# Kernel tuning notes

Measured on AMD Instinct MI355X. Metric: run time of the kernel, lower is better.

Reference implementation:

```python
import jax, jax.numpy as jnp
import numpy as np

B, L, D, H = 64, 64, 512, 512


def setup_inputs() -> dict:
    key = jax.random.key(0)
    ks = jax.random.split(key, 6)
    x = jax.random.normal(ks[0], (B, L, D), dtype=jnp.float32)
    length = jax.random.randint(ks[1], (B,), L // 2, L + 1)  # in [L/2, L]
    # torch Linear convention: weight (out_features, in_features)
    w_word = jax.random.normal(ks[2], (2 * H, D), dtype=jnp.float32) * (1.0 / np.sqrt(D))
    b_word = jnp.zeros((2 * H,), dtype=jnp.float32)
    w_comp = jax.random.normal(ks[3], (5 * H, 2 * H), dtype=jnp.float32) * (1.0 / np.sqrt(2 * H))
    b_comp = jnp.zeros((5 * H,), dtype=jnp.float32)
    comp_query = jax.random.normal(ks[4], (H,), dtype=jnp.float32) * 0.01
    return {"x": x, "length": length, "w_word": w_word, "b_word": b_word,
            "w_comp": w_comp, "b_comp": b_comp, "comp_query": comp_query}


def _treelstm_cell(hl, cl, hr, cr, w_comp, b_comp):
    v = jnp.concatenate([hl, hr], axis=2) @ w_comp.T + b_comp  # (B, n, 5H)
    i, fl, fr, u, o = jnp.split(v, 5, axis=2)
    c = (cl * jax.nn.sigmoid(fl + 1.0) + cr * jax.nn.sigmoid(fr + 1.0)
         + jnp.tanh(u) * jax.nn.sigmoid(i))
    h = jax.nn.sigmoid(o) * jnp.tanh(c)
    return h, c


def _forward(x, length, w_word, b_word, w_comp, b_comp, comp_query):
    max_depth = x.shape[1]
    hdim = comp_query.shape[0]
    # length_mask[b, t] = t < length[b]
    length_mask = (jnp.arange(max_depth)[None, :] < length[:, None]).astype(x.dtype)
    state = x @ w_word.T + b_word  # (B, L, 2H)
    h, c = jnp.split(state, 2, axis=2)
    NEG = jnp.asarray(-1e9, dtype=x.dtype)
    for i in range(max_depth - 1):
        hl, cl = h[:, :-1, :], c[:, :-1, :]
        hr, cr = h[:, 1:, :], c[:, 1:, :]
        new_h, new_c = _treelstm_cell(hl, cl, hr, cr, w_comp, b_comp)
        if i < max_depth - 2:
            # greedy merge-point selection (eval-mode greedy_select)
            cw = jnp.einsum('bnh,h->bn', new_h, comp_query) / np.sqrt(hdim)
            m = length_mask[:, i + 1:]  # (B, L-1-i)
            logits = jnp.where(m > 0, cw, NEG)
            sel = jax.nn.one_hot(jnp.argmax(logits, axis=1), logits.shape[1], dtype=x.dtype)
            cs = jnp.cumsum(sel, axis=1)
            left = (1.0 - cs)[:, :, None]
            right = (cs - sel)[:, :, None]
            s = sel[:, :, None]
            new_h = s * new_h + left * hl + right * hr
            new_c = s * new_c + left * cl + right * cr
        done = length_mask[:, i + 1][:, None, None]
        h = done * new_h + (1.0 - done) * h[:, :-1, :]
        c = done * new_c + (1.0 - done) * c[:, :-1, :]
    return h[:, 0, :], c[:, 0, :]


def reference(x, length, w_word, b_word, w_comp, b_comp, comp_query):
    return _forward(x, length, w_word, b_word, w_comp, b_comp, comp_query)
```

## Files before the change

kernel.cpp:

```cpp
#include <hip/hip_runtime.h>

typedef __bf16 bf16;
typedef short s16x8 __attribute__((ext_vector_type(8)));
typedef float f32x4 __attribute__((ext_vector_type(4)));
typedef unsigned long long u64;

#define MFMA16(a, b, c) __builtin_amdgcn_mfma_f32_16x16x32_bf16((a), (b), (c), 0, 0, 0)
#define NROW 187
#define UROW 251

__device__ __forceinline__ float sigf(float x) { return 1.0f / (1.0f + expf(-x)); }
__device__ __forceinline__ s16x8 ld8(const bf16* p) { return *(const s16x8*)p; }

__device__ __forceinline__ unsigned packhl(float v) {
    bf16 h = (bf16)v;
    bf16 l = (bf16)(v - (float)h);
    return (unsigned)__builtin_bit_cast(unsigned short, h) |
           ((unsigned)__builtin_bit_cast(unsigned short, l) << 16);
}
__device__ __forceinline__ u64 lda64(const unsigned* p) {
    return __hip_atomic_load((const u64*)p, __ATOMIC_RELAXED, __HIP_MEMORY_SCOPE_AGENT);
}
__device__ __forceinline__ u64 lda64u(const u64* p) {
    return __hip_atomic_load(p, __ATOMIC_RELAXED, __HIP_MEMORY_SCOPE_AGENT);
}
__device__ __forceinline__ void stau64(u64* p, u64 v) {
    __hip_atomic_store(p, v, __ATOMIC_RELAXED, __HIP_MEMORY_SCOPE_AGENT);
}
__device__ __forceinline__ unsigned lda32(const unsigned* p) {
    return __hip_atomic_load(p, __ATOMIC_RELAXED, __HIP_MEMORY_SCOPE_AGENT);
}
__device__ __forceinline__ float ldaf(const float* p) {
    return __hip_atomic_load(p, __ATOMIC_RELAXED, __HIP_MEMORY_SCOPE_AGENT);
}
__device__ __forceinline__ void staf(float* p, float v) {
    __hip_atomic_store(p, v, __ATOMIC_RELAXED, __HIP_MEMORY_SCOPE_AGENT);
}
__device__ __forceinline__ void stau(unsigned* p, unsigned v) {
    __hip_atomic_store(p, v, __ATOMIC_RELAXED, __HIP_MEMORY_SCOPE_AGENT);
}

__device__ bf16  g_xhi[64 * 64 * 512], g_xlo[64 * 64 * 512];
__device__ bf16  g_wwhi[1024 * 512], g_wwlo[1024 * 512];
__device__ bf16  g_wchi[2560 * 1024], g_wclo[2560 * 1024];
__device__ bf16  g_hhi[64 * 64 * 512];
__device__ bf16  g_hlo[64 * 64 * 512];
__device__ unsigned g_uhl[(size_t)64 * UROW * 512];
__device__ float g_uc[(size_t)64 * UROW * 512];
__device__ float g_spinit[64 * 63 * 32];
__device__ u64   g_spart2[2 * 128 * 32];
__device__ unsigned g_flag[63 * 8 * 32];

__global__ __launch_bounds__(256) void k_prep(const float* __restrict__ x,
                                              const float* __restrict__ ww,
                                              const float* __restrict__ wc) {
    const int NX = 64 * 64 * 512, NW = 1024 * 512, NC = 2560 * 1024;
    int stride = gridDim.x * 256, i0 = blockIdx.x * 256 + threadIdx.x;
    for (int i = i0; i < NX; i += stride) {
        float v = x[i];
        bf16 h = (bf16)v;
        g_xhi[i] = h;
        g_xlo[i] = (bf16)(v - (float)h);
    }
    for (int i = i0; i < NW; i += stride) {
        float v = ww[i];
        bf16 h = (bf16)v;
        g_wwhi[i] = h;
        g_wwlo[i] = (bf16)(v - (float)h);
    }
    for (int i = i0; i < NC; i += stride) {
        float v = wc[i];
        bf16 h = (bf16)v;
        g_wchi[i] = h;
        g_wclo[i] = (bf16)(v - (float)h);
    }
}

__global__ __launch_bounds__(64) void k_leaf(const float* __restrict__ b_word) {
    int cg = blockIdx.x, rg = blockIdx.y;
    int lane = threadIdx.x, l15 = lane & 15, quad = lane >> 4;
    const bf16* axh = g_xhi + (size_t)(rg * 16 + l15) * 512;
    const bf16* axl = g_xlo + (size_t)(rg * 16 + l15) * 512;
    const bf16* bwh = g_wwhi + (size_t)(cg * 64 + l15) * 512;
    const bf16* bwl = g_wwlo + (size_t)(cg * 64 + l15) * 512;
    f32x4 acc[4] = {};
    for (int kc = 0; kc < 16; ++kc) {
        int k = kc * 32 + quad * 8;
        s16x8 aH = ld8(axh + k), aL = ld8(axl + k);
#pragma unroll
        for (int t = 0; t < 4; ++t) {
            s16x8 bH = ld8(bwh + (size_t)t * 16 * 512 + k);
            s16x8 bL = ld8(bwl + (size_t)t * 16 * 512 + k);
            acc[t] = MFMA16(aH, bH, acc[t]);
            acc[t] = MFMA16(aH, bL, acc[t]);
            acc[t] = MFMA16(aL, bH, acc[t]);
        }
    }
#pragma unroll
    for (int t = 0; t < 4; ++t) {
        int col = cg * 64 + t * 16 + l15;
        float bw = b_word[col];
#pragma unroll
        for (int r = 0; r < 4; ++r) {
            int m = rg * 16 + quad * 4 + r;
            int bb = m >> 6, sl = m & 63;
            float v = acc[t][r] + bw;
            if (col < 512) {
                bf16 hi = (bf16)v;
                g_hhi[(size_t)m * 512 + col] = hi;
                g_hlo[(size_t)m * 512 + col] = (bf16)(v - (float)hi);
                g_uhl[((size_t)bb * UROW + sl) * 512 + col] = packhl(v);
            } else {
                g_uc[((size_t)bb * UROW + sl) * 512 + (col - 512)] = v;
            }
        }
    }
}

__global__ __launch_bounds__(64) void k_cells_init(const int* __restrict__ length,
                                                   const float* __restrict__ b_comp,
                                                   const float* __restrict__ q) {
    int fg = blockIdx.x;
    int rg = blockIdx.y;
    int lane = threadIdx.x, l15 = lane & 15, quad = lane >> 4;

    const bf16 *ahi[4], *alo[4];
#pragma unroll
    for (int t = 0; t < 4; ++t) {
        int r = rg * 64 + t * 16 + l15;
        int b = r / 63, j = r - b * 63;
        ahi[t] = g_hhi + (size_t)(b * 64 + j) * 512;
        alo[t] = g_hlo + (size_t)(b * 64 + j) * 512;
    }
    const bf16* wh = g_wchi + (size_t)(fg * 16 + l15) * 1024;
    const bf16* wl = g_wclo + (size_t)(fg * 16 + l15) * 1024;
    f32x4 acc[4][5] = {};
    for (int kc = 0; kc < 32; ++kc) {
        int k = kc * 32 + quad * 8;
        int kk = k & 511;
        size_t sh = (k < 512) ? 0 : 512;
        s16x8 aH[4], aL[4];
#pragma unroll
        for (int t = 0; t < 4; ++t) {
            aH[t] = ld8(ahi[t] + sh + kk);
            aL[t] = ld8(alo[t] + sh + kk);
        }
#pragma unroll
        for (int g = 0; g < 5; ++g) {
            s16x8 bH = ld8(wh + (size_t)g * 512 * 1024 + k);
            s16x8 bL = ld8(wl + (size_t)g * 512 * 1024 + k);
#pragma unroll
            for (int t = 0; t < 4; ++t) {
                acc[t][g] = MFMA16(aH[t], bH, acc[t][g]);
                acc[t][g] = MFMA16(aH[t], bL, acc[t][g]);
                acc[t][g] = MFMA16(aL[t], bH, acc[t][g]);
            }
        }
    }
    int col = fg * 16 + l15;
    float bc[5];
#pragma unroll
    for (int g = 0; g < 5; ++g) bc[g] = b_comp[g * 512 + col];
    float qv = q[col];
#pragma unroll
    for (int t = 0; t < 4; ++t) {
#pragma unroll
        for (int rr = 0; rr < 4; ++rr) {
            int R = rg * 64 + t * 16 + quad * 4 + rr;
            int B_ = R / 63, J = R - B_ * 63;
            bool act = (J <= length[B_] - 2);
            float gi = acc[t][0][rr] + bc[0];
            float fl = acc[t][1][rr] + bc[1];
            float fr = acc[t][2][rr] + bc[2];
            float gu = acc[t][3][rr] + bc[3];
            float go = acc[t][4][rr] + bc[4];
            float cl = g_uc[((size_t)B_ * UROW + J) * 512 + col];
            float cr = g_uc[((size_t)B_ * UROW + J + 1) * 512 + col];
            float cn = cl * sigf(fl + 1.0f) + cr * sigf(fr + 1.0f) + tanhf(gu) * sigf(gi);
            float hn = sigf(go) * tanhf(cn);
            float sp = hn * qv;
#pragma unroll
            for (int off = 1; off < 16; off <<= 1) sp += __shfl_xor(sp, off, 16);
            if (act) {
                size_t o = ((size_t)B_ * UROW + 64 + J) * 512 + col;
                g_uhl[o] = packhl(hn);
                g_uc[o] = cn;
                if (l15 == 0) g_spinit[(size_t)R * 32 + fg] = sp;
            }
        }
    }
}

__global__ __launch_bounds__(256, 1) void k_loop_p(const int* __restrict__ length,
                                                   const float* __restrict__ b_comp,
                                                   const float* __restrict__ q,
                                                   float* __restrict__ out) {
    int fg = blockIdx.x, rg = blockIdx.y;
    int tid = threadIdx.x;
    int wv = tid >> 6, lane = tid & 63;
    int l15 = lane & 15, quad = lane >> 4;
    const float sqrt_h = 22.627416997969522f;

    __shared__ int s_next[8][64], s_prev[8][64], s_aliv[8][64];
    __shared__ int s_enc[8][64];
    __shared__ int s_prow[8][64];
    __shared__ float s_score[8][64];
    __shared__ int s_np[8][2];
    __shared__ int s_dl[16], s_dr[16], s_dd[16];
    __shared__ int s_len[8];
    __shared__ float s_red[4][64][21];

    for (int bl = wv * 2; bl < wv * 2 + 2; ++bl) {
        int b = rg * 8 + bl;
        int len = length[b];
        if (lane == 0) { s_len[bl] = len; s_np[bl][0] = -1; s_np[bl][1] = -1; }
        s_next[bl][lane] = (lane < len - 1) ? lane + 1 : -1;
        s_prev[bl][lane] = (lane > 0 && lane < len) ? lane - 1 : -1;
        s_aliv[bl][lane] = (lane < len) ? 1 : 0;
        s_enc[bl][lane] = lane;
        s_prow[bl][lane] = lane;
        float sc = -3.0e38f;
        if (lane < 63 && lane <= len - 2) {
            float s = 0.0f;
            for (int f = 0; f < 32; ++f) s += g_spinit[(size_t)(b * 63 + lane) * 32 + f];
            sc = s / sqrt_h;
        }
        s_score[bl][lane] = sc;
    }
    __syncthreads();

    int col = fg * 16 + l15;
    float bc[5];
#pragma unroll
    for (int g = 0; g < 5; ++g) bc[g] = b_comp[g * 512 + col];
    float qv = q[col];
    const bf16* wh = g_wchi + (size_t)col * 1024;
    const bf16* wl = g_wclo + (size_t)col * 1024;

    s16x8 rbH[8][5], rbL[8][5];
#pragma unroll
    for (int i = 0; i < 8; ++i) {
        int k = (wv * 8 + i) * 32 + quad * 8;
#pragma unroll
        for (int g = 0; g < 5; ++g) {
            rbH[i][g] = ld8(wh + (size_t)g * 512 * 1024 + k);
            rbL[i][g] = ld8(wl + (size_t)g * 512 * 1024 + k);
        }
    }

    for (int it = 0; it < 63; ++it) {
        for (int bl = wv * 2; bl < wv * 2 + 2; ++bl) {
            int len = s_len[bl];
            int r0 = bl * 2;
            bool active = (it <= len - 2);
            if (!active) {
                if (lane == 0) {
                    s_dl[r0] = 0; s_dr[r0] = 1; s_dd[r0] = -1;
                    s_dl[r0 + 1] = 0; s_dr[r0 + 1] = 1; s_dd[r0 + 1] = -1;
                }
                continue;
            }
            if (it > 0) {
                int s = lane >> 5, f = lane & 31;
                int p = s_np[bl][s];
                float v = 0.0f;
                if (p >= 0) {
                    const u64* sl = &g_spart2[((size_t)((it - 1) & 1) * 128
                                              + rg * 16 + r0 + s) * 32 + f];
                    u64 w = lda64u(sl);
                    while ((unsigned)(w >> 32) != (unsigned)it) {
                        __builtin_amdgcn_s_sleep(1);
                        w = lda64u(sl);
                    }
                    v = __builtin_bit_cast(float, (unsigned)(w & 0xffffffffu));
                }
#pragma unroll
                for (int off = 1; off < 32; off <<= 1) v += __shfl_xor(v, off, 32);
                if (f == 0 && p >= 0) s_score[bl][p] = v / sqrt_h;
            }
            float val = -3.0e38f;
            int idx = lane;
            if (lane < 63 && s_aliv[bl][lane] && s_next[bl][lane] >= 0)
                val = s_score[bl][lane];
#pragma unroll
            for (int off = 1; off < 64; off <<= 1) {
                float ov = __shfl_xor(val, off, 64);
                int oi = __shfl_xor(idx, off, 64);
                if (ov > val || (ov == val && oi < idx)) { val = ov; idx = oi; }
            }
            int a = idx;
            if (a < 0) a = 0;
            if (a > 62) a = 62;
            if (lane == 0) {
                int bn = s_next[bl][a];
                int nn = (bn >= 0) ? s_next[bl][bn] : -1;
                s_next[bl][a] = nn;
                if (nn >= 0) s_prev[bl][nn] = a;
                if (bn >= 0) s_aliv[bl][bn] = 0;
                s_enc[bl][a] = 64 + s_prow[bl][a];
                int pL = s_prev[bl][a];
                int pR = (nn >= 0) ? a : -1;
                s_np[bl][0] = pL;
                s_np[bl][1] = pR;
                if (pL >= 0) {
                    s_dl[r0] = s_enc[bl][pL]; s_dr[r0] = s_enc[bl][a];
                    s_dd[r0] = 63 + 2 * it;  s_prow[bl][pL] = 63 + 2 * it;
                } else { s_dl[r0] = 0; s_dr[r0] = 1; s_dd[r0] = -1; }
                if (pR >= 0) {
                    s_dl[r0 + 1] = s_enc[bl][a]; s_dr[r0 + 1] = s_enc[bl][nn];
                    s_dd[r0 + 1] = 63 + 2 * it + 1; s_prow[bl][a] = 63 + 2 * it + 1;
                } else { s_dl[r0 + 1] = 0; s_dr[r0 + 1] = 1; s_dd[r0 + 1] = -1; }
            }
        }
        __syncthreads();
        if (it > 0) {
            const unsigned* fp = &g_flag[((size_t)(it - 1) * 8 + rg) * 32];
            for (;;) {
                unsigned fv = lda32(fp + (lane & 31));
                if (__all(fv != 0)) break;
                __builtin_amdgcn_s_sleep(1);
            }
            __atomic_signal_fence(__ATOMIC_SEQ_CST);
        }
        if (it < 62) {
            int b_r = rg * 8 + (l15 >> 1);
            const unsigned* la = g_uhl + ((size_t)b_r * UROW + s_dl[l15]) * 512;
            const unsigned* ra = g_uhl + ((size_t)b_r * UROW + s_dr[l15]) * 512;
            const unsigned* base = (wv < 2) ? la : ra;

            u64 ub[32];
#pragma unroll
            for (int i = 0; i < 8; ++i) {
                int kk = ((wv * 8 + i) * 32 + quad * 8) & 511;
                const unsigned* ap = base + kk;
                ub[4 * i + 0] = lda64(ap);
                ub[4 * i + 1] = lda64(ap + 2);
                ub[4 * i + 2] = lda64(ap + 4);
                ub[4 * i + 3] = lda64(ap + 6);
            }
            int rowm = quad * 4 + wv;
            int bb = rg * 8 + (rowm >> 1);
            float clv = ldaf(&g_uc[((size_t)bb * UROW + s_dl[rowm]) * 512 + col]);
            float crv = ldaf(&g_uc[((size_t)bb * UROW + s_dr[rowm]) * 512 + col]);

            f32x4 acc[5] = {};
#pragma unroll
            for (int i = 0; i < 8; ++i) {
                u64 u0 = ub[4 * i + 0], u1 = ub[4 * i + 1];
                u64 u2 = ub[4 * i + 2], u3 = ub[4 * i + 3];
                s16x8 aH, aL;
                aH[0] = (short)u0; aL[0] = (short)(u0 >> 16);
                aH[1] = (short)(u0 >> 32); aL[1] = (short)(u0 >> 48);
                aH[2] = (short)u1; aL[2] = (short)(u1 >> 16);
                aH[3] = (short)(u1 >> 32); aL[3] = (short)(u1 >> 48);
                aH[4] = (short)u2; aL[4] = (short)(u2 >> 16);
                aH[5] = (short)(u2 >> 32); aL[5] = (short)(u2 >> 48);
                aH[6] = (short)u3; aL[6] = (short)(u3 >> 16);
                aH[7] = (short)(u3 >> 32); aL[7] = (short)(u3 >> 48);
#pragma unroll
                for (int g = 0; g < 5; ++g) {
                    acc[g] = MFMA16(aH, rbH[i][g], acc[g]);
                    acc[g] = MFMA16(aH, rbL[i][g], acc[g]);
                    acc[g] = MFMA16(aL, rbH[i][g], acc[g]);
                }
            }
#pragma unroll
            for (int g = 0; g < 5; ++g)
#pragma unroll
                for (int rr = 0; rr < 4; ++rr)
                    s_red[wv][lane][g * 4 + rr] = acc[g][rr];
            __syncthreads();
            {
                float accs[5];
#pragma unroll
                for (int g = 0; g < 5; ++g)
                    accs[g] = ((s_red[0][lane][g * 4 + wv] + s_red[1][lane][g * 4 + wv])
                               + s_red[2][lane][g * 4 + wv]) + s_red[3][lane][g * 4 + wv];
                int dest = s_dd[rowm];
                float gi = accs[0] + bc[0];
                float fl = accs[1] + bc[1];
                float fr = accs[2] + bc[2];
                float gu = accs[3] + bc[3];
                float go = accs[4] + bc[4];
                float cn = clv * sigf(fl + 1.0f) + crv * sigf(fr + 1.0f)
                           + tanhf(gu) * sigf(gi);
                float hn = sigf(go) * tanhf(cn);
                float sp = hn * qv;
#pragma unroll
                for (int off = 1; off < 16; off <<= 1) sp += __shfl_xor(sp, off, 16);
                if (dest >= 0) {
                    if (l15 == 0) {
                        u64 w = ((u64)(unsigned)(it + 1) << 32)
                                | (u64)__builtin_bit_cast(unsigned, sp);
                        stau64(&g_spart2[((size_t)(it & 1) * 128
                                         + rg * 16 + rowm) * 32 + fg], w);
                    }
                    size_t o = ((size_t)bb * UROW + 64 + dest) * 512 + col;
                    stau(&g_uhl[o], packhl(hn));
                    staf(&g_uc[o], cn);
                }
            }
            __builtin_amdgcn_s_waitcnt(0);
            __syncthreads();
            if (tid == 0)
                stau(&g_flag[((size_t)it * 8 + rg) * 32 + fg], 1u);
        }
    }
    if (wv == 0) {
        __builtin_amdgcn_s_waitcnt(0);
        for (int bl = 0; bl < 8; ++bl) {
            if ((lane >> 4) != (bl & 3)) continue;
            int b = rg * 8 + bl;
            int e0 = s_enc[bl][0];
            unsigned u = lda32(&g_uhl[((size_t)b * UROW + e0) * 512 + col]);
            bf16 h0 = __builtin_bit_cast(bf16, (unsigned short)(u & 0xffffu));
            bf16 l0 = __builtin_bit_cast(bf16, (unsigned short)(u >> 16));
            float hv = (float)h0 + (float)l0;
            float cv = ldaf(&g_uc[((size_t)b * UROW + e0) * 512 + col]);
            out[(size_t)b * 512 + col] = hv;
            out[(size_t)(64 * 512) + b * 512 + col] = cv;
        }
    }
}

extern "C" void kernel_launch(void* const* d_in, const int* in_sizes, int n_in,
                              void* d_out, int out_size, void* d_ws, size_t ws_size,
                              hipStream_t stream) {
    const float* x = (const float*)d_in[0];
    const int* length = (const int*)d_in[1];
    const float* w_word = (const float*)d_in[2];
    const float* b_word = (const float*)d_in[3];
    const float* w_comp = (const float*)d_in[4];
    const float* b_comp = (const float*)d_in[5];
    const float* q = (const float*)d_in[6];
    float* out = (float*)d_out;

    unsigned* flagp;
    hipGetSymbolAddress((void**)&flagp, HIP_SYMBOL(g_flag));
    hipMemsetAsync(flagp, 0, 63 * 8 * 32 * sizeof(unsigned), stream);
    u64* sp2p;
    hipGetSymbolAddress((void**)&sp2p, HIP_SYMBOL(g_spart2));
    hipMemsetAsync(sp2p, 0, 2 * 128 * 32 * sizeof(u64), stream);

    hipLaunchKernelGGL(k_prep, dim3(2048), dim3(256), 0, stream, x, w_word, w_comp);
    hipLaunchKernelGGL(k_leaf, dim3(16, 256), dim3(64), 0, stream, b_word);
    hipLaunchKernelGGL(k_cells_init, dim3(32, 63), dim3(64), 0, stream,
                       length, b_comp, q);

    hipLaunchKernelGGL(k_loop_p, dim3(32, 8), dim3(256), 0, stream,
                       length, b_comp, q, out);
}
```

Measured before the change: 880.9 us.

## Restructure initial cell GEMM with register-resident weights and split-K across waves

The first tree-LSTM cell kernel now keeps each block's weight slice in registers, splits the K dimension across four waves and reduces the partial sums through shared memory. It loops over 32 row chunks per block, on a 32x8 grid instead of 32x63 single-wave blocks. Activations are read from the packed hi/lo g_uhl buffer, so the separate g_hhi/g_hlo arrays and the leaf kernel's writes to them are removed. The aim is to stop reloading weights per tile and cut leaf-kernel stores, at the cost of heavy register pressure, two block barriers per chunk and fewer blocks in flight.

```diff
diff --git a/kernel.cpp b/kernel.cpp
--- a/kernel.cpp
+++ b/kernel.cpp
@@ -43,8 +43,6 @@
 __device__ bf16  g_xhi[64 * 64 * 512], g_xlo[64 * 64 * 512];
 __device__ bf16  g_wwhi[1024 * 512], g_wwlo[1024 * 512];
 __device__ bf16  g_wchi[2560 * 1024], g_wclo[2560 * 1024];
-__device__ bf16  g_hhi[64 * 64 * 512];
-__device__ bf16  g_hlo[64 * 64 * 512];
 __device__ unsigned g_uhl[(size_t)64 * UROW * 512];
 __device__ float g_uc[(size_t)64 * UROW * 512];
 __device__ float g_spinit[64 * 63 * 32];
@@ -106,9 +104,6 @@
             int bb = m >> 6, sl = m & 63;
             float v = acc[t][r] + bw;
             if (col < 512) {
-                bf16 hi = (bf16)v;
-                g_hhi[(size_t)m * 512 + col] = hi;
-                g_hlo[(size_t)m * 512 + col] = (bf16)(v - (float)hi);
                 g_uhl[((size_t)bb * UROW + sl) * 512 + col] = packhl(v);
             } else {
                 g_uc[((size_t)bb * UROW + sl) * 512 + (col - 512)] = v;
@@ -117,77 +112,115 @@
     }
 }
 
-__global__ __launch_bounds__(64) void k_cells_init(const int* __restrict__ length,
-                                                   const float* __restrict__ b_comp,
-                                                   const float* __restrict__ q) {
-    int fg = blockIdx.x;
-    int rg = blockIdx.y;
-    int lane = threadIdx.x, l15 = lane & 15, quad = lane >> 4;
-
-    const bf16 *ahi[4], *alo[4];
-#pragma unroll
-    for (int t = 0; t < 4; ++t) {
-        int r = rg * 64 + t * 16 + l15;
-        int b = r / 63, j = r - b * 63;
-        ahi[t] = g_hhi + (size_t)(b * 64 + j) * 512;
-        alo[t] = g_hlo + (size_t)(b * 64 + j) * 512;
-    }
-    const bf16* wh = g_wchi + (size_t)(fg * 16 + l15) * 1024;
-    const bf16* wl = g_wclo + (size_t)(fg * 16 + l15) * 1024;
-    f32x4 acc[4][5] = {};
-    for (int kc = 0; kc < 32; ++kc) {
-        int k = kc * 32 + quad * 8;
-        int kk = k & 511;
-        size_t sh = (k < 512) ? 0 : 512;
-        s16x8 aH[4], aL[4];
-#pragma unroll
-        for (int t = 0; t < 4; ++t) {
-            aH[t] = ld8(ahi[t] + sh + kk);
-            aL[t] = ld8(alo[t] + sh + kk);
-        }
-#pragma unroll
-        for (int g = 0; g < 5; ++g) {
-            s16x8 bH = ld8(wh + (size_t)g * 512 * 1024 + k);
-            s16x8 bL = ld8(wl + (size_t)g * 512 * 1024 + k);
-#pragma unroll
-            for (int t = 0; t < 4; ++t) {
-                acc[t][g] = MFMA16(aH[t], bH, acc[t][g]);
-                acc[t][g] = MFMA16(aH[t], bL, acc[t][g]);
-                acc[t][g] = MFMA16(aL[t], bH, acc[t][g]);
-            }
-        }
-    }
+__global__ __launch_bounds__(256, 1) void k_cells_init(const int* __restrict__ length,
+                                                       const float* __restrict__ b_comp,
+                                                       const float* __restrict__ q) {
+    int fg = blockIdx.x, bg = blockIdx.y;
+    int tid = threadIdx.x;
+    int wv = tid >> 6, lane = tid & 63;
+    int l15 = lane & 15, quad = lane >> 4;
+
+    __shared__ float s_red[4][64][21];
+    __shared__ int s_len[8];
+    if (tid < 8) s_len[tid] = length[bg * 8 + tid];
+    __syncthreads();
+
     int col = fg * 16 + l15;
     float bc[5];
 #pragma unroll
     for (int g = 0; g < 5; ++g) bc[g] = b_comp[g * 512 + col];
     float qv = q[col];
-#pragma unroll
-    for (int t = 0; t < 4; ++t) {
-#pragma unroll
-        for (int rr = 0; rr < 4; ++rr) {
-            int R = rg * 64 + t * 16 + quad * 4 + rr;
-            int B_ = R / 63, J = R - B_ * 63;
-            bool act = (J <= length[B_] - 2);
-            float gi = acc[t][0][rr] + bc[0];
-            float fl = acc[t][1][rr] + bc[1];
-            float fr = acc[t][2][rr] + bc[2];
-            float gu = acc[t][3][rr] + bc[3];
-            float go = acc[t][4][rr] + bc[4];
-            float cl = g_uc[((size_t)B_ * UROW + J) * 512 + col];
-            float cr = g_uc[((size_t)B_ * UROW + J + 1) * 512 + col];
-            float cn = cl * sigf(fl + 1.0f) + cr * sigf(fr + 1.0f) + tanhf(gu) * sigf(gi);
+    const bf16* wh = g_wchi + (size_t)col * 1024;
+    const bf16* wl = g_wclo + (size_t)col * 1024;
+
+    s16x8 rbH[8][5], rbL[8][5];
+#pragma unroll
+    for (int i = 0; i < 8; ++i) {
+        int k = (wv * 8 + i) * 32 + quad * 8;
+#pragma unroll
+        for (int g = 0; g < 5; ++g) {
+            rbH[i][g] = ld8(wh + (size_t)g * 512 * 1024 + k);
+            rbL[i][g] = ld8(wl + (size_t)g * 512 * 1024 + k);
+        }
+    }
+
+    for (int ch = 0; ch < 32; ++ch) {
+        int r = ch * 16 + l15;
+        int rv = (r < 504) ? r : 0;
+        int lb = rv / 63, j = rv - lb * 63;
+        const unsigned* base = g_uhl + ((size_t)(bg * 8 + lb) * UROW + j) * 512
+                               + ((wv < 2) ? 0 : 512);
+        u64 ub[32];
+#pragma unroll
+        for (int i = 0; i < 8; ++i) {
+            int kk = ((wv * 8 + i) * 32 + quad * 8) & 511;
+            const unsigned* ap = base + kk;
+            ub[4 * i + 0] = lda64(ap);
+            ub[4 * i + 1] = lda64(ap + 2);
+            ub[4 * i + 2] = lda64(ap + 4);
+            ub[4 * i + 3] = lda64(ap + 6);
+        }
+        int rowm = quad * 4 + wv;
+        int r2 = ch * 16 + rowm;
+        int rv2 = (r2 < 504) ? r2 : 0;
+        int lb2 = rv2 / 63, j2 = rv2 - lb2 * 63;
+        int b2 = bg * 8 + lb2;
+        float clv = g_uc[((size_t)b2 * UROW + j2) * 512 + col];
+        float crv = g_uc[((size_t)b2 * UROW + j2 + 1) * 512 + col];
+        bool act = (r2 < 504) && (j2 <= s_len[lb2] - 2);
+
+        f32x4 acc[5] = {};
+#pragma unroll
+        for (int i = 0; i < 8; ++i) {
+            u64 u0 = ub[4 * i + 0], u1 = ub[4 * i + 1];
+            u64 u2 = ub[4 * i + 2], u3 = ub[4 * i + 3];
+            s16x8 aH, aL;
+            aH[0] = (short)u0; aL[0] = (short)(u0 >> 16);
+            aH[1] = (short)(u0 >> 32); aL[1] = (short)(u0 >> 48);
+            aH[2] = (short)u1; aL[2] = (short)(u1 >> 16);
+            aH[3] = (short)(u1 >> 32); aL[3] = (short)(u1 >> 48);
+            aH[4] = (short)u2; aL[4] = (short)(u2 >> 16);
+            aH[5] = (short)(u2 >> 32); aL[5] = (short)(u2 >> 48);
+            aH[6] = (short)u3; aL[6] = (short)(u3 >> 16);
+            aH[7] = (short)(u3 >> 32); aL[7] = (short)(u3 >> 48);
+#pragma unroll
+            for (int g = 0; g < 5; ++g) {
+                acc[g] = MFMA16(aH, rbH[i][g], acc[g]);
+                acc[g] = MFMA16(aH, rbL[i][g], acc[g]);
+                acc[g] = MFMA16(aL, rbH[i][g], acc[g]);
+            }
+        }
+#pragma unroll
+        for (int g = 0; g < 5; ++g)
+#pragma unroll
+            for (int rr = 0; rr < 4; ++rr)
+                s_red[wv][lane][g * 4 + rr] = acc[g][rr];
+        __syncthreads();
+        {
+            float accs[5];
+#pragma unroll
+            for (int g = 0; g < 5; ++g)
+                accs[g] = ((s_red[0][lane][g * 4 + wv] + s_red[1][lane][g * 4 + wv])
+                           + s_red[2][lane][g * 4 + wv]) + s_red[3][lane][g * 4 + wv];
+            float gi = accs[0] + bc[0];
+            float fl = accs[1] + bc[1];
+            float fr = accs[2] + bc[2];
+            float gu = accs[3] + bc[3];
+            float go = accs[4] + bc[4];
+            float cn = clv * sigf(fl + 1.0f) + crv * sigf(fr + 1.0f)
+                       + tanhf(gu) * sigf(gi);
             float hn = sigf(go) * tanhf(cn);
             float sp = hn * qv;
 #pragma unroll
             for (int off = 1; off < 16; off <<= 1) sp += __shfl_xor(sp, off, 16);
             if (act) {
-                size_t o = ((size_t)B_ * UROW + 64 + J) * 512 + col;
+                size_t o = ((size_t)b2 * UROW + 64 + j2) * 512 + col;
                 g_uhl[o] = packhl(hn);
                 g_uc[o] = cn;
-                if (l15 == 0) g_spinit[(size_t)R * 32 + fg] = sp;
-            }
-        }
+                if (l15 == 0) g_spinit[((size_t)b2 * 63 + j2) * 32 + fg] = sp;
+            }
+        }
+        __syncthreads();
     }
 }
 
@@ -444,7 +477,7 @@
 
     hipLaunchKernelGGL(k_prep, dim3(2048), dim3(256), 0, stream, x, w_word, w_comp);
     hipLaunchKernelGGL(k_leaf, dim3(16, 256), dim3(64), 0, stream, b_word);
-    hipLaunchKernelGGL(k_cells_init, dim3(32, 63), dim3(64), 0, stream,
+    hipLaunchKernelGGL(k_cells_init, dim3(32, 8), dim3(256), 0, stream,
                        length, b_comp, q);
 
     hipLaunchKernelGGL(k_loop_p, dim3(32, 8), dim3(256), 0, stream,
```

New measurement: 907.9 us (median of 2 runs). +3.1%, slower.
